# Optimization experiments

Measured on AMD Instinct MI355X. Metric: run time of the kernel, lower is better.

Reference implementation:

```python
import jax, jax.numpy as jnp
import numpy as np

B = 1024          # graphs
NPG = 258         # nodes per graph (hard-coded in the model's reshape)
N = B * NPG
F_IN = 64
DEG = 8
E = B * NPG * DEG
CH = 32
HID = 128


def setup_inputs() -> dict:
    key = jax.random.key(0)
    ks = jax.random.split(key, 16)
    x = jax.random.normal(ks[0], (N, F_IN), dtype=jnp.float32)
    # within-graph random edges (disjoint batch): local idx in [0,258) + graph offset
    src_l = jax.random.randint(ks[1], (E,), 0, NPG, dtype=jnp.int32)
    dst_l = jax.random.randint(ks[2], (E,), 0, NPG, dtype=jnp.int32)
    offs = jnp.repeat(jnp.arange(B, dtype=jnp.int32) * NPG, NPG * DEG)
    edge_src = src_l + offs
    edge_dst = dst_l + offs
    edge_w = jax.random.uniform(ks[3], (E,), dtype=jnp.float32)
    s = lambda f: 1.0 / np.sqrt(f)
    W0 = jax.random.normal(ks[4], (F_IN, CH), dtype=jnp.float32) * s(F_IN)
    W1 = jax.random.normal(ks[5], (F_IN, CH), dtype=jnp.float32) * s(F_IN)
    b_conv = jnp.zeros((CH,), dtype=jnp.float32)
    Wd1 = jax.random.normal(ks[6], (NPG * CH, HID), dtype=jnp.float32) * s(NPG * CH)
    bd1 = jnp.zeros((HID,), dtype=jnp.float32)
    Wd2 = jax.random.normal(ks[7], (HID, HID // 2), dtype=jnp.float32) * s(HID)
    bd2 = jnp.zeros((HID // 2,), dtype=jnp.float32)
    Wd3 = jax.random.normal(ks[8], (HID // 2, HID // 4), dtype=jnp.float32) * s(HID // 2)
    bd3 = jnp.zeros((HID // 4,), dtype=jnp.float32)
    Wd4 = jax.random.normal(ks[9], (HID // 4, 1), dtype=jnp.float32) * s(HID // 4)
    bd4 = jnp.zeros((1,), dtype=jnp.float32)
    return dict(x=x, edge_src=edge_src, edge_dst=edge_dst, edge_w=edge_w,
                W0=W0, W1=W1, b_conv=b_conv, Wd1=Wd1, bd1=bd1, Wd2=Wd2, bd2=bd2,
                Wd3=Wd3, bd3=bd3, Wd4=Wd4, bd4=bd4)


def reference(x, edge_src, edge_dst, edge_w, W0, W1, b_conv,
              Wd1, bd1, Wd2, bd2, Wd3, bd3, Wd4, bd4):
    n = x.shape[0]
    # ChebConv K=2: T0 = X, T1 = A_hat X ; out = T0 W0 + T1 W1 + b, elu
    ax = jax.ops.segment_sum(edge_w[:, None] * x[edge_src], edge_dst, num_segments=n)
    h = jax.nn.elu(x @ W0 + ax @ W1 + b_conv)          # [N, 32]
    h = h.reshape(n // NPG, NPG * CH)                   # [B, 258*32] (reshape+flatten)
    h = jax.nn.relu(h @ Wd1 + bd1)
    h = jax.nn.relu(h @ Wd2 + bd2)
    # dropout is inactive at inference
    h = jax.nn.relu(h @ Wd3 + bd3)
    out = jax.nn.sigmoid(h @ Wd4 + bd4)                 # [B, 1]
    return out
```

## Files before the change

kernel.cpp:

```cpp
#include <hip/hip_runtime.h>
#include <hip/hip_bf16.h>

#define NPG 258
#define DEG 8
#define EPG 2064
#define CH 32
#define FIN 64
#define NB 1024
#define NTOT (NB * NPG)
#define HID 128
#define KTOT 8256
#define KSPL 32

typedef __attribute__((ext_vector_type(8))) short bf16x8;
typedef __attribute__((ext_vector_type(4))) float f32x4;

__device__ inline unsigned short f2bf(float f) {
    __hip_bfloat16 b = __float2bfloat16(f);
    return __builtin_bit_cast(unsigned short, b);
}
__device__ inline float bf2f(unsigned short u) {
    return __builtin_bit_cast(float, (unsigned)u << 16);
}
__device__ inline void cvt_split(const float4 a, const float4 b, bf16x8& hi, bf16x8& lo) {
    float f[8] = {a.x, a.y, a.z, a.w, b.x, b.y, b.z, b.w};
#pragma unroll
    for (int j = 0; j < 8; ++j) {
        unsigned short h = f2bf(f[j]);
        hi[j] = (short)h;
        lo[j] = (short)f2bf(f[j] - bf2f(h));
    }
}

__global__ __launch_bounds__(256) void prep(
    const float* __restrict__ W0, const float* __restrict__ W1,
    unsigned short* __restrict__ Wh, unsigned short* __restrict__ Wl,
    const float* __restrict__ Wd1, unsigned short* __restrict__ Wd1T)
{
    const int tid = threadIdx.x;
    if (blockIdx.x == 0) {
#pragma unroll
        for (int i = 0; i < 16; ++i) {
            const int idx = tid + i * 256;
            const int c = idx >> 6, k = idx & 63;
            const float v = (c < 32) ? W0[k * CH + c] : W1[k * CH + (c - 32)];
            const unsigned short h = f2bf(v);
            Wh[c * 64 + k] = h;
            Wl[c * 64 + k] = f2bf(v - bf2f(h));
        }
        return;
    }
    __shared__ float st[128][65];
    const int k0 = (blockIdx.x - 1) * 64;
#pragma unroll
    for (int i = 0; i < 32; ++i) {
        const int idx = tid + i * 256;
        const int kl = idx >> 7, cc = idx & 127;
        st[cc][kl] = Wd1[(size_t)(k0 + kl) * HID + cc];
    }
    __syncthreads();
    const int cc = tid >> 1, gq = tid & 1;
#pragma unroll
    for (int i = 0; i < 8; ++i) {
        const int ko = (gq + i * 2) * 4;
        ushort4 o;
        o.x = f2bf(st[cc][ko + 0]);
        o.y = f2bf(st[cc][ko + 1]);
        o.z = f2bf(st[cc][ko + 2]);
        o.w = f2bf(st[cc][ko + 3]);
        *reinterpret_cast<ushort4*>(Wd1T + (size_t)cc * KTOT + k0 + ko) = o;
    }
}

__global__ __launch_bounds__(512, 4) void conv_fused(
    const float* __restrict__ x, const int* __restrict__ esrc,
    const int* __restrict__ edst, const float* __restrict__ ew,
    const unsigned short* __restrict__ Wh, const unsigned short* __restrict__ Wl,
    const float* __restrict__ bc, unsigned short* __restrict__ h)
{
    __shared__ float          y0s[NPG * CH];
    __shared__ unsigned short y1s[NPG * CH];
    __shared__ unsigned short bsh[64 * 64];
    __shared__ unsigned short bsl[64 * 64];
    __shared__ unsigned short slot_src[EPG];
    __shared__ float          slot_w[EPG];
    __shared__ int            row_start[NPG + 1];
    __shared__ int            cursor[NPG];

    const int g   = blockIdx.x;
    const int tid = threadIdx.x;
    const int n0  = g * NPG;
    const long eb = (long)g * EPG;
    const long qb = (long)g * (NPG * CH);

    {
        const int col = tid >> 3, o = tid & 7;
        const int so = o ^ (col & 7);
        *reinterpret_cast<uint4*>(&bsh[col * 64 + so * 8]) =
            *reinterpret_cast<const uint4*>(&Wh[col * 64 + o * 8]);
        *reinterpret_cast<uint4*>(&bsl[col * 64 + so * 8]) =
            *reinterpret_cast<const uint4*>(&Wl[col * 64 + o * 8]);
    }
    if (tid < NPG) cursor[tid] = 0;
    __syncthreads();

    unsigned e_u[4];
    float    e_wv[4];
#pragma unroll
    for (int i = 0; i < 4; ++i) {
        const int e = tid + i * 512;
        const int sl = esrc[eb + e] - n0;
        const int dl = edst[eb + e] - n0;
        e_u[i] = (unsigned)sl | ((unsigned)dl << 16);
        e_wv[i] = ew[eb + e];
        atomicAdd(&cursor[dl], 1);
    }
    unsigned e_u4 = 0; float e_w4 = 0.f;
    const bool has4 = (tid < EPG - 2048);
    if (has4) {
        const int e = tid + 2048;
        const int sl = esrc[eb + e] - n0;
        const int dl = edst[eb + e] - n0;
        e_u4 = (unsigned)sl | ((unsigned)dl << 16);
        e_w4 = ew[eb + e];
        atomicAdd(&cursor[dl], 1);
    }

    const int w = tid >> 6, lane = tid & 63;
    const int r = lane & 15, kq = lane >> 4;
    for (int t = w; t < 17; t += 8) {
        const int rbase = t * 16;
        const int rowc = min(rbase + r, NPG - 1);
        const float* xp = x + (long)(n0 + rowc) * FIN + kq * 8;
        bf16x8 ah[2], al[2];
#pragma unroll
        for (int ks = 0; ks < 2; ++ks) {
            const float4 p0 = *reinterpret_cast<const float4*>(xp + ks * 32);
            const float4 p1 = *reinterpret_cast<const float4*>(xp + ks * 32 + 4);
            cvt_split(p0, p1, ah[ks], al[ks]);
        }
        f32x4 acc[4];
#pragma unroll
        for (int nt = 0; nt < 4; ++nt) acc[nt] = f32x4{0.f, 0.f, 0.f, 0.f};
#pragma unroll
        for (int nt = 0; nt < 4; ++nt) {
            const int col = nt * 16 + r;
            const int cs = col & 7;
#pragma unroll
            for (int ks = 0; ks < 2; ++ks) {
                const int gg = (ks * 4 + kq) ^ cs;
                const bf16x8 bh = *reinterpret_cast<const bf16x8*>(&bsh[col * 64 + gg * 8]);
                const bf16x8 bl = *reinterpret_cast<const bf16x8*>(&bsl[col * 64 + gg * 8]);
                acc[nt] = __builtin_amdgcn_mfma_f32_16x16x32_bf16(ah[ks], bh, acc[nt], 0, 0, 0);
                acc[nt] = __builtin_amdgcn_mfma_f32_16x16x32_bf16(ah[ks], bl, acc[nt], 0, 0, 0);
                acc[nt] = __builtin_amdgcn_mfma_f32_16x16x32_bf16(al[ks], bh, acc[nt], 0, 0, 0);
            }
        }
#pragma unroll
        for (int rr = 0; rr < 4; ++rr) {
            const int row = rbase + kq * 4 + rr;
            if (row < NPG) {
                y0s[row * CH + r]      = acc[0][rr];
                y0s[row * CH + 16 + r] = acc[1][rr];
                y1s[row * CH + r]      = f2bf(acc[2][rr]);
                y1s[row * CH + 16 + r] = f2bf(acc[3][rr]);
            }
        }
    }
    __syncthreads();

    if (tid < 64) {
        const int b0 = tid * 5;
        int loc[5], s = 0;
#pragma unroll
        for (int j = 0; j < 5; ++j) {
            const int idx = b0 + j;
            loc[j] = (idx < NPG) ? cursor[idx] : 0;
            s += loc[j];
        }
        int inc = s;
#pragma unroll
        for (int off = 1; off < 64; off <<= 1) {
            const int tshf = __shfl_up(inc, off, 64);
            if (tid >= off) inc += tshf;
        }
        int run = inc - s;
#pragma unroll
        for (int j = 0; j < 5; ++j) {
            const int idx = b0 + j;
            if (idx < NPG) { row_start[idx] = run; cursor[idx] = run; }
            run += loc[j];
        }
        if (tid == 63) row_start[NPG] = inc;
    }
    __syncthreads();

#pragma unroll
    for (int i = 0; i < 4; ++i) {
        const int dl = e_u[i] >> 16;
        const int pos = atomicAdd(&cursor[dl], 1);
        slot_src[pos] = (unsigned short)(e_u[i] & 0xFFFFu);
        slot_w[pos] = e_wv[i];
    }
    if (has4) {
        const int dl = e_u4 >> 16;
        const int pos = atomicAdd(&cursor[dl], 1);
        slot_src[pos] = (unsigned short)(e_u4 & 0xFFFFu);
        slot_w[pos] = e_w4;
    }
    __syncthreads();

    const int grp = tid >> 4;
    const int c = (tid & 15) * 2;
    const float b0 = bc[c], b1 = bc[c + 1];
#pragma unroll 1
    for (int p = 0; p < 9; ++p) {
        const int n = p * 32 + grp;
        if (n >= NPG) break;
        const int pb = row_start[n], pe = row_start[n + 1];
        float a0 = 0.f, a1 = 0.f;
        for (int pos = pb; pos < pe; ++pos) {
            const float wv = slot_w[pos];
            const unsigned u = *reinterpret_cast<const unsigned*>(
                &y1s[slot_src[pos] * CH + c]);
            a0 += wv * bf2f((unsigned short)(u & 0xFFFFu));
            a1 += wv * bf2f((unsigned short)(u >> 16));
        }
        float v0 = y0s[n * CH + c] + b0 + a0;
        float v1 = y0s[n * CH + c + 1] + b1 + a1;
        v0 = (v0 > 0.f) ? v0 : expm1f(v0);
        v1 = (v1 > 0.f) ? v1 : expm1f(v1);
        const unsigned o = (unsigned)f2bf(v0) | ((unsigned)f2bf(v1) << 16);
        *reinterpret_cast<unsigned*>(&h[qb + (long)n * CH + c]) = o;
    }
}

__global__ __launch_bounds__(256) void gemm1(
    const unsigned short* __restrict__ h, const unsigned short* __restrict__ Wd1T,
    float* __restrict__ part)
{
    const int tid = threadIdx.x, w = tid >> 6, lane = tid & 63;
    const int r = lane & 15, kq = lane >> 4;
    const long m0 = (long)blockIdx.x * 64;
    const int ks = blockIdx.y;
    const int kb0 = ks * 258 / KSPL, kb1 = (ks + 1) * 258 / KSPL;
    const int c0 = w * 32;

    f32x4 acc[4][2];
#pragma unroll
    for (int a = 0; a < 4; ++a)
#pragma unroll
        for (int b = 0; b < 2; ++b) acc[a][b] = f32x4{0.f, 0.f, 0.f, 0.f};

    const unsigned short* ap = h    + (m0 + r) * KTOT + kq * 8;
    const unsigned short* bp = Wd1T + (long)(c0 + r) * KTOT + kq * 8;

    for (int kb = kb0; kb < kb1; ++kb) {
        const int k = kb * 32;
        const bf16x8 b0 = *reinterpret_cast<const bf16x8*>(bp + k);
        const bf16x8 b1 = *reinterpret_cast<const bf16x8*>(bp + 16 * KTOT + k);
#pragma unroll
        for (int mt = 0; mt < 4; ++mt) {
            const bf16x8 a = *reinterpret_cast<const bf16x8*>(ap + mt * 16 * KTOT + k);
            acc[mt][0] = __builtin_amdgcn_mfma_f32_16x16x32_bf16(a, b0, acc[mt][0], 0, 0, 0);
            acc[mt][1] = __builtin_amdgcn_mfma_f32_16x16x32_bf16(a, b1, acc[mt][1], 0, 0, 0);
        }
    }

    float* p = part + ((long)ks * NB + m0) * HID + c0;
#pragma unroll
    for (int mt = 0; mt < 4; ++mt)
#pragma unroll
        for (int rr = 0; rr < 4; ++rr) {
            const int row = mt * 16 + kq * 4 + rr;
            p[(long)row * HID + r]      = acc[mt][0][rr];
            p[(long)row * HID + 16 + r] = acc[mt][1][rr];
        }
}

__global__ __launch_bounds__(256) void mlp_tail(
    const float* __restrict__ part, const float* __restrict__ bd1,
    const float* __restrict__ Wd2, const float* __restrict__ bd2,
    const float* __restrict__ Wd3, const float* __restrict__ bd3,
    const float* __restrict__ Wd4, const float* __restrict__ bd4,
    float* __restrict__ out)
{
    __shared__ float w2[128 * 64];
    __shared__ float w3[64 * 32];
    __shared__ float w4[32];
    __shared__ float h1s[4][128];
    __shared__ float h2s[4][64];
    __shared__ float h3s[4][32];

    const int tid = threadIdx.x;
    for (int i = tid; i < 128 * 64; i += 256) w2[i] = Wd2[i];
    for (int i = tid; i < 64 * 32; i += 256)  w3[i] = Wd3[i];
    if (tid < 32) w4[tid] = Wd4[tid];

    const int r = tid >> 6;
    const int lane = tid & 63;
    const int row = blockIdx.x * 4 + r;

    float s0 = bd1[lane], s1 = bd1[lane + 64];
#pragma unroll 8
    for (int s = 0; s < KSPL; ++s) {
        const float* p = part + ((long)s * NB + row) * HID;
        s0 += p[lane];
        s1 += p[lane + 64];
    }
    h1s[r][lane]      = fmaxf(s0, 0.f);
    h1s[r][lane + 64] = fmaxf(s1, 0.f);
    __syncthreads();

    float s2 = bd2[lane];
#pragma unroll 8
    for (int k = 0; k < 128; ++k) s2 += h1s[r][k] * w2[k * 64 + lane];
    h2s[r][lane] = fmaxf(s2, 0.f);
    __syncthreads();

    if (lane < 32) {
        float s3 = bd3[lane];
#pragma unroll 8
        for (int k = 0; k < 64; ++k) s3 += h2s[r][k] * w3[k * 32 + lane];
        h3s[r][lane] = fmaxf(s3, 0.f);
    }
    __syncthreads();

    float p4 = (lane < 32) ? h3s[r][lane] * w4[lane] : 0.f;
#pragma unroll
    for (int off = 32; off > 0; off >>= 1) p4 += __shfl_down(p4, off, 64);
    if (lane == 0) out[row] = 1.f / (1.f + expf(-(p4 + bd4[0])));
}

extern "C" void kernel_launch(void* const* d_in, const int* in_sizes, int n_in,
                              void* d_out, int out_size, void* d_ws, size_t ws_size,
                              hipStream_t stream)
{
    const float* x    = (const float*)d_in[0];
    const int*   esrc = (const int*)d_in[1];
    const int*   edst = (const int*)d_in[2];
    const float* ew   = (const float*)d_in[3];
    const float* W0   = (const float*)d_in[4];
    const float* W1   = (const float*)d_in[5];
    const float* bc   = (const float*)d_in[6];
    const float* Wd1  = (const float*)d_in[7];
    const float* bd1  = (const float*)d_in[8];
    const float* Wd2  = (const float*)d_in[9];
    const float* bd2  = (const float*)d_in[10];
    const float* Wd3  = (const float*)d_in[11];
    const float* bd3  = (const float*)d_in[12];
    const float* Wd4  = (const float*)d_in[13];
    const float* bd4  = (const float*)d_in[14];
    float* out = (float*)d_out;

    char* wsb = (char*)d_ws;
    unsigned short* h    = (unsigned short*)wsb;
    unsigned short* wd1t = (unsigned short*)(wsb + 16908288);
    unsigned short* wch  = (unsigned short*)(wsb + 19021824);
    unsigned short* wcl  = (unsigned short*)(wsb + 19030016);
    float*          part = (float*)(wsb + 19038208);

    prep<<<1 + KTOT / 64, 256, 0, stream>>>(W0, W1, wch, wcl, Wd1, wd1t);
    conv_fused<<<NB, 512, 0, stream>>>(x, esrc, edst, ew, wch, wcl, bc, h);
    gemm1<<<dim3(NB / 64, KSPL), 256, 0, stream>>>(h, wd1t, part);
    mlp_tail<<<NB / 4, 256, 0, stream>>>(part, bd1, Wd2, bd2, Wd3, bd3, Wd4, bd4, out);
}
```

Measured before the change: 196.9 us.

## Fuse dense GEMM with MLP tail, shrink conv LDS, drop second atomic pass

The split-K gemm1 and mlp_tail kernels are replaced by a single dense_fused kernel. Each of its 64 blocks computes 16 rows over the full K dimension and then runs the small MLP layers in LDS, which removes the partial-sum round trip through global memory. In conv_fused, y0 is stored as bf16, the weight and slot buffers share one LDS region, and edge slots come from the first atomic pass instead of a second atomic pass, so the kernel can target 6 blocks per CU. Risks: only 64 blocks run the dense GEMM with long serial K loops, which means low parallelism. Storing y0 in bf16 also loses precision.

```diff
diff --git a/kernel.cpp b/kernel.cpp
--- a/kernel.cpp
+++ b/kernel.cpp
@@ -10,7 +10,6 @@
 #define NTOT (NB * NPG)
 #define HID 128
 #define KTOT 8256
-#define KSPL 32
 
 typedef __attribute__((ext_vector_type(8))) short bf16x8;
 typedef __attribute__((ext_vector_type(4))) float f32x4;
@@ -72,20 +71,22 @@
     }
 }
 
-__global__ __launch_bounds__(512, 4) void conv_fused(
+__global__ __launch_bounds__(512, 6) void conv_fused(
     const float* __restrict__ x, const int* __restrict__ esrc,
     const int* __restrict__ edst, const float* __restrict__ ew,
     const unsigned short* __restrict__ Wh, const unsigned short* __restrict__ Wl,
     const float* __restrict__ bc, unsigned short* __restrict__ h)
 {
-    __shared__ float          y0s[NPG * CH];
+    __shared__ unsigned short y0s[NPG * CH];
     __shared__ unsigned short y1s[NPG * CH];
-    __shared__ unsigned short bsh[64 * 64];
-    __shared__ unsigned short bsl[64 * 64];
-    __shared__ unsigned short slot_src[EPG];
-    __shared__ float          slot_w[EPG];
-    __shared__ int            row_start[NPG + 1];
-    __shared__ int            cursor[NPG];
+    __shared__ __align__(16) char wbuf[16384];
+    __shared__ int row_start[NPG + 1];
+    __shared__ int cursor[NPG];
+
+    unsigned short* bsh = (unsigned short*)wbuf;
+    unsigned short* bsl = bsh + 4096;
+    unsigned short* slot_src = (unsigned short*)wbuf;
+    float*          slot_w   = (float*)(wbuf + 4128);
 
     const int g   = blockIdx.x;
     const int tid = threadIdx.x;
@@ -106,6 +107,7 @@
 
     unsigned e_u[4];
     float    e_wv[4];
+    int      e_p[4];
 #pragma unroll
     for (int i = 0; i < 4; ++i) {
         const int e = tid + i * 512;
@@ -113,9 +115,9 @@
         const int dl = edst[eb + e] - n0;
         e_u[i] = (unsigned)sl | ((unsigned)dl << 16);
         e_wv[i] = ew[eb + e];
-        atomicAdd(&cursor[dl], 1);
-    }
-    unsigned e_u4 = 0; float e_w4 = 0.f;
+        e_p[i] = atomicAdd(&cursor[dl], 1);
+    }
+    unsigned e_u4 = 0; float e_w4 = 0.f; int e_p4 = 0;
     const bool has4 = (tid < EPG - 2048);
     if (has4) {
         const int e = tid + 2048;
@@ -123,7 +125,7 @@
         const int dl = edst[eb + e] - n0;
         e_u4 = (unsigned)sl | ((unsigned)dl << 16);
         e_w4 = ew[eb + e];
-        atomicAdd(&cursor[dl], 1);
+        e_p4 = atomicAdd(&cursor[dl], 1);
     }
 
     const int w = tid >> 6, lane = tid & 63;
@@ -160,8 +162,8 @@
         for (int rr = 0; rr < 4; ++rr) {
             const int row = rbase + kq * 4 + rr;
             if (row < NPG) {
-                y0s[row * CH + r]      = acc[0][rr];
-                y0s[row * CH + 16 + r] = acc[1][rr];
+                y0s[row * CH + r]      = f2bf(acc[0][rr]);
+                y0s[row * CH + 16 + r] = f2bf(acc[1][rr]);
                 y1s[row * CH + r]      = f2bf(acc[2][rr]);
                 y1s[row * CH + 16 + r] = f2bf(acc[3][rr]);
             }
@@ -188,7 +190,7 @@
 #pragma unroll
         for (int j = 0; j < 5; ++j) {
             const int idx = b0 + j;
-            if (idx < NPG) { row_start[idx] = run; cursor[idx] = run; }
+            if (idx < NPG) row_start[idx] = run;
             run += loc[j];
         }
         if (tid == 63) row_start[NPG] = inc;
@@ -197,16 +199,14 @@
 
 #pragma unroll
     for (int i = 0; i < 4; ++i) {
-        const int dl = e_u[i] >> 16;
-        const int pos = atomicAdd(&cursor[dl], 1);
-        slot_src[pos] = (unsigned short)(e_u[i] & 0xFFFFu);
-        slot_w[pos] = e_wv[i];
+        const int slot = row_start[e_u[i] >> 16] + e_p[i];
+        slot_src[slot] = (unsigned short)(e_u[i] & 0xFFFFu);
+        slot_w[slot] = e_wv[i];
     }
     if (has4) {
-        const int dl = e_u4 >> 16;
-        const int pos = atomicAdd(&cursor[dl], 1);
-        slot_src[pos] = (unsigned short)(e_u4 & 0xFFFFu);
-        slot_w[pos] = e_w4;
+        const int slot = row_start[e_u4 >> 16] + e_p4;
+        slot_src[slot] = (unsigned short)(e_u4 & 0xFFFFu);
+        slot_w[slot] = e_w4;
     }
     __syncthreads();
 
@@ -219,15 +219,20 @@
         if (n >= NPG) break;
         const int pb = row_start[n], pe = row_start[n + 1];
         float a0 = 0.f, a1 = 0.f;
+        int us = (pb < pe) ? slot_src[pb] : 0;
+        float wv = (pb < pe) ? slot_w[pb] : 0.f;
         for (int pos = pb; pos < pe; ++pos) {
-            const float wv = slot_w[pos];
-            const unsigned u = *reinterpret_cast<const unsigned*>(
-                &y1s[slot_src[pos] * CH + c]);
+            const int nx = pos + 1;
+            const int us2 = (nx < pe) ? slot_src[nx] : 0;
+            const float wv2 = (nx < pe) ? slot_w[nx] : 0.f;
+            const unsigned u = *reinterpret_cast<const unsigned*>(&y1s[us * CH + c]);
             a0 += wv * bf2f((unsigned short)(u & 0xFFFFu));
             a1 += wv * bf2f((unsigned short)(u >> 16));
-        }
-        float v0 = y0s[n * CH + c] + b0 + a0;
-        float v1 = y0s[n * CH + c + 1] + b1 + a1;
+            us = us2; wv = wv2;
+        }
+        const unsigned u0 = *reinterpret_cast<const unsigned*>(&y0s[n * CH + c]);
+        float v0 = bf2f((unsigned short)(u0 & 0xFFFFu)) + b0 + a0;
+        float v1 = bf2f((unsigned short)(u0 >> 16)) + b1 + a1;
         v0 = (v0 > 0.f) ? v0 : expm1f(v0);
         v1 = (v1 > 0.f) ? v1 : expm1f(v1);
         const unsigned o = (unsigned)f2bf(v0) | ((unsigned)f2bf(v1) << 16);
@@ -235,101 +240,92 @@
     }
 }
 
-__global__ __launch_bounds__(256) void gemm1(
+__global__ __launch_bounds__(512, 2) void dense_fused(
     const unsigned short* __restrict__ h, const unsigned short* __restrict__ Wd1T,
-    float* __restrict__ part)
+    const float* __restrict__ bd1, const float* __restrict__ Wd2,
+    const float* __restrict__ bd2, const float* __restrict__ Wd3,
+    const float* __restrict__ bd3, const float* __restrict__ Wd4,
+    const float* __restrict__ bd4, float* __restrict__ out)
 {
-    const int tid = threadIdx.x, w = tid >> 6, lane = tid & 63;
+    __shared__ unsigned short As[16][264];
+    __shared__ float h1s[16][128];
+    __shared__ float w2s[128 * 64];
+    __shared__ float w3s[64 * 32];
+    __shared__ float w4s[32];
+    __shared__ float h2s[16][64];
+    __shared__ float h3s[16][32];
+
+    const int tid = threadIdx.x;
+    const long m0 = (long)blockIdx.x * 16;
+    const int w = tid >> 6, lane = tid & 63;
     const int r = lane & 15, kq = lane >> 4;
-    const long m0 = (long)blockIdx.x * 64;
-    const int ks = blockIdx.y;
-    const int kb0 = ks * 258 / KSPL, kb1 = (ks + 1) * 258 / KSPL;
-    const int c0 = w * 32;
-
-    f32x4 acc[4][2];
-#pragma unroll
-    for (int a = 0; a < 4; ++a)
-#pragma unroll
-        for (int b = 0; b < 2; ++b) acc[a][b] = f32x4{0.f, 0.f, 0.f, 0.f};
-
-    const unsigned short* ap = h    + (m0 + r) * KTOT + kq * 8;
+    const int c0 = w * 16;
+
+    for (int i = tid; i < 128 * 64; i += 512) w2s[i] = Wd2[i];
+    for (int i = tid; i < 64 * 32; i += 512)  w3s[i] = Wd3[i];
+    if (tid < 32) w4s[tid] = Wd4[tid];
+
+    f32x4 acc = {0.f, 0.f, 0.f, 0.f};
     const unsigned short* bp = Wd1T + (long)(c0 + r) * KTOT + kq * 8;
-
-    for (int kb = kb0; kb < kb1; ++kb) {
-        const int k = kb * 32;
-        const bf16x8 b0 = *reinterpret_cast<const bf16x8*>(bp + k);
-        const bf16x8 b1 = *reinterpret_cast<const bf16x8*>(bp + 16 * KTOT + k);
-#pragma unroll
-        for (int mt = 0; mt < 4; ++mt) {
-            const bf16x8 a = *reinterpret_cast<const bf16x8*>(ap + mt * 16 * KTOT + k);
-            acc[mt][0] = __builtin_amdgcn_mfma_f32_16x16x32_bf16(a, b0, acc[mt][0], 0, 0, 0);
-            acc[mt][1] = __builtin_amdgcn_mfma_f32_16x16x32_bf16(a, b1, acc[mt][1], 0, 0, 0);
-        }
-    }
-
-    float* p = part + ((long)ks * NB + m0) * HID + c0;
-#pragma unroll
-    for (int mt = 0; mt < 4; ++mt)
-#pragma unroll
-        for (int rr = 0; rr < 4; ++rr) {
-            const int row = mt * 16 + kq * 4 + rr;
-            p[(long)row * HID + r]      = acc[mt][0][rr];
-            p[(long)row * HID + 16 + r] = acc[mt][1][rr];
-        }
-}
-
-__global__ __launch_bounds__(256) void mlp_tail(
-    const float* __restrict__ part, const float* __restrict__ bd1,
-    const float* __restrict__ Wd2, const float* __restrict__ bd2,
-    const float* __restrict__ Wd3, const float* __restrict__ bd3,
-    const float* __restrict__ Wd4, const float* __restrict__ bd4,
-    float* __restrict__ out)
-{
-    __shared__ float w2[128 * 64];
-    __shared__ float w3[64 * 32];
-    __shared__ float w4[32];
-    __shared__ float h1s[4][128];
-    __shared__ float h2s[4][64];
-    __shared__ float h3s[4][32];
-
-    const int tid = threadIdx.x;
-    for (int i = tid; i < 128 * 64; i += 256) w2[i] = Wd2[i];
-    for (int i = tid; i < 64 * 32; i += 256)  w3[i] = Wd3[i];
-    if (tid < 32) w4[tid] = Wd4[tid];
-
-    const int r = tid >> 6;
-    const int lane = tid & 63;
-    const int row = blockIdx.x * 4 + r;
-
-    float s0 = bd1[lane], s1 = bd1[lane + 64];
+    const int arow = tid >> 5, aseg = tid & 31;
+
+    for (int ch = 0; ch < 32; ++ch) {
+        const int k0 = ch * 256;
+        __syncthreads();
+        *reinterpret_cast<uint4*>(&As[arow][aseg * 8]) =
+            *reinterpret_cast<const uint4*>(&h[(m0 + arow) * KTOT + k0 + aseg * 8]);
+        __syncthreads();
+#pragma unroll
+        for (int kb = 0; kb < 8; ++kb) {
+            const bf16x8 a = *reinterpret_cast<const bf16x8*>(&As[r][kb * 32 + kq * 8]);
+            const bf16x8 b = *reinterpret_cast<const bf16x8*>(bp + k0 + kb * 32);
+            acc = __builtin_amdgcn_mfma_f32_16x16x32_bf16(a, b, acc, 0, 0, 0);
+        }
+    }
+    __syncthreads();
+    if (tid < 128) {
+        const int row = tid >> 3, seg = tid & 7;
+        *reinterpret_cast<uint4*>(&As[row][seg * 8]) =
+            *reinterpret_cast<const uint4*>(&h[(m0 + row) * KTOT + 8192 + seg * 8]);
+    }
+    __syncthreads();
+#pragma unroll
+    for (int kb = 0; kb < 2; ++kb) {
+        const bf16x8 a = *reinterpret_cast<const bf16x8*>(&As[r][kb * 32 + kq * 8]);
+        const bf16x8 b = *reinterpret_cast<const bf16x8*>(bp + 8192 + kb * 32);
+        acc = __builtin_amdgcn_mfma_f32_16x16x32_bf16(a, b, acc, 0, 0, 0);
+    }
+
+    const float b1v = bd1[c0 + r];
+#pragma unroll
+    for (int rr = 0; rr < 4; ++rr)
+        h1s[kq * 4 + rr][c0 + r] = fmaxf(acc[rr] + b1v, 0.f);
+    __syncthreads();
+
+    for (int idx = tid; idx < 16 * 64; idx += 512) {
+        const int rr = idx >> 6, j = idx & 63;
+        float s = bd2[j];
 #pragma unroll 8
-    for (int s = 0; s < KSPL; ++s) {
-        const float* p = part + ((long)s * NB + row) * HID;
-        s0 += p[lane];
-        s1 += p[lane + 64];
-    }
-    h1s[r][lane]      = fmaxf(s0, 0.f);
-    h1s[r][lane + 64] = fmaxf(s1, 0.f);
-    __syncthreads();
-
-    float s2 = bd2[lane];
+        for (int k = 0; k < 128; ++k) s += h1s[rr][k] * w2s[k * 64 + j];
+        h2s[rr][j] = fmaxf(s, 0.f);
+    }
+    __syncthreads();
+
+    {
+        const int rr = tid >> 5, j = tid & 31;
+        float s = bd3[j];
 #pragma unroll 8
-    for (int k = 0; k < 128; ++k) s2 += h1s[r][k] * w2[k * 64 + lane];
-    h2s[r][lane] = fmaxf(s2, 0.f);
-    __syncthreads();
-
-    if (lane < 32) {
-        float s3 = bd3[lane];
-#pragma unroll 8
-        for (int k = 0; k < 64; ++k) s3 += h2s[r][k] * w3[k * 32 + lane];
-        h3s[r][lane] = fmaxf(s3, 0.f);
-    }
-    __syncthreads();
-
-    float p4 = (lane < 32) ? h3s[r][lane] * w4[lane] : 0.f;
-#pragma unroll
-    for (int off = 32; off > 0; off >>= 1) p4 += __shfl_down(p4, off, 64);
-    if (lane == 0) out[row] = 1.f / (1.f + expf(-(p4 + bd4[0])));
+        for (int k = 0; k < 64; ++k) s += h2s[rr][k] * w3s[k * 32 + j];
+        h3s[rr][j] = fmaxf(s, 0.f);
+    }
+    __syncthreads();
+
+    if (tid < 16) {
+        float s = 0.f;
+#pragma unroll
+        for (int k = 0; k < 32; ++k) s += h3s[tid][k] * w4s[k];
+        out[m0 + tid] = 1.f / (1.f + expf(-(s + bd4[0])));
+    }
 }
 
 extern "C" void kernel_launch(void* const* d_in, const int* in_sizes, int n_in,
@@ -358,10 +354,8 @@
     unsigned short* wd1t = (unsigned short*)(wsb + 16908288);
     unsigned short* wch  = (unsigned short*)(wsb + 19021824);
     unsigned short* wcl  = (unsigned short*)(wsb + 19030016);
-    float*          part = (float*)(wsb + 19038208);
 
     prep<<<1 + KTOT / 64, 256, 0, stream>>>(W0, W1, wch, wcl, Wd1, wd1t);
     conv_fused<<<NB, 512, 0, stream>>>(x, esrc, edst, ew, wch, wcl, bc, h);
-    gemm1<<<dim3(NB / 64, KSPL), 256, 0, stream>>>(h, wd1t, part);
-    mlp_tail<<<NB / 4, 256, 0, stream>>>(part, bd1, Wd2, bd2, Wd3, bd3, Wd4, bd4, out);
-}
+    dense_fused<<<NB / 16, 512, 0, stream>>>(h, wd1t, bd1, Wd2, bd2, Wd3, bd3, Wd4, bd4, out);
+}
```

After: 316.9 us. 61.0% more time.
